# Kernel tuning notes

Hardware: AMD Instinct MI355X
Metric: run time of the kernel (lower is better)

Reference implementation:

```python
import math
import jax, jax.numpy as jnp
from jax import lax
import numpy as np

E = 16        # num experts
K = 2         # top_k
CF = 1.25     # capacity factor


def setup_inputs() -> dict:
    key = jax.random.key(0)
    k0, k1, k2, k3, k4 = jax.random.split(key, 5)
    B, S, D, H = 2, 2048, 1024, 1024
    scale = 0.02
    return {
        "x": jax.random.normal(k0, (B, S, D), dtype=jnp.float32),
        "router_w": jax.random.normal(k1, (D, E), dtype=jnp.float32) * scale,
        "gate_w": jax.random.normal(k2, (E, D, H), dtype=jnp.float32) * scale,
        "up_w": jax.random.normal(k3, (E, D, H), dtype=jnp.float32) * scale,
        "down_w": jax.random.normal(k4, (E, H, D), dtype=jnp.float32) * scale,
    }


def reference(x, router_w, gate_w, up_w, down_w):
    B, S, D = x.shape
    xf = x.reshape(-1, D)                     # [T, D]
    T = B * S
    capacity = max(1, math.ceil(T * K / E * CF))   # static python int
    Cbuf = K * capacity                       # per-expert buffer (per-column capacity x K)

    # ---- router: softmax over experts, then top-k (weights = top-k probs) ----
    logits = xf @ router_w                    # [T, E]
    probs = jax.nn.softmax(logits, axis=-1)
    w, idx = lax.top_k(probs, K)              # [T, K] each

    # ---- capacity drop: per k-column, per expert, keep first `capacity` tokens ----
    oh = jax.nn.one_hot(idx, E, dtype=w.dtype)            # [T, K, E]
    rank = jnp.cumsum(oh, axis=0) - oh                     # exclusive rank per (k, e)
    myrank = jnp.sum(rank * oh, axis=-1)                   # [T, K]
    keep = myrank < capacity
    w = jnp.where(keep, w, 0.0)

    # ---- dispatch: scatter kept assignments into [E, Cbuf] slots ----
    flat_e = idx.reshape(-1)                               # [A], A = T*K (row-major: token-major)
    flat_w = w.reshape(-1)
    keep_f = keep.reshape(-1)
    tok = jnp.repeat(jnp.arange(T, dtype=jnp.int32), K)    # [A]
    ohk = jax.nn.one_hot(flat_e, E, dtype=jnp.int32) * keep_f[:, None].astype(jnp.int32)
    pos = jnp.cumsum(ohk, axis=0) - ohk                    # exclusive rank among kept per expert
    slot = jnp.sum(pos * ohk, axis=-1)                     # [A], < Cbuf for kept
    e_idx = jnp.where(keep_f, flat_e, E)                   # dropped -> dummy expert row E

    dispatch = jnp.full((E + 1, Cbuf), T, dtype=jnp.int32).at[e_idx, slot].set(tok)
    wbuf = jnp.zeros((E + 1, Cbuf), dtype=w.dtype).at[e_idx, slot].set(flat_w)
    dispatch = dispatch[:E]
    wbuf = wbuf[:E]

    x_pad = jnp.concatenate([xf, jnp.zeros((1, D), xf.dtype)], axis=0)  # sentinel row
    xe = x_pad[dispatch]                                   # [E, Cbuf, D]

    # ---- grouped SwiGLU expert GEMMs ----
    gate = jnp.einsum('ecd,edh->ech', xe, gate_w)
    up = jnp.einsum('ecd,edh->ech', xe, up_w)
    hidden = jax.nn.silu(gate) * up
    out = jnp.einsum('ech,ehd->ecd', hidden, down_w)       # [E, Cbuf, D]
    out = out * wbuf[:, :, None]

    # ---- combine: scatter-add back to tokens ----
    combined = jnp.zeros((T + 1, D), dtype=xf.dtype).at[dispatch.reshape(-1)].add(out.reshape(-1, D))
    return combined[:T].reshape(B, S, D)
```

## Files before the change

### kernel.cpp

```cpp
#include <hip/hip_runtime.h>
#include <math.h>

#define T_TOK 4096
#define DIM   1024
#define HID   1024
#define NE    16
#define CAP   640
#define CBUF  1280
#define BM 128
#define BN 64
#define BK 32
#define MAXTILE 160

typedef __attribute__((ext_vector_type(8))) short short8;
typedef __attribute__((ext_vector_type(4))) float f32x4;

static __device__ __forceinline__ unsigned short f2bf(float f) {
    unsigned int u = __float_as_uint(f);
    u += 0x7fff + ((u >> 16) & 1);
    return (unsigned short)(u >> 16);
}

#define PICK4(v,i) ((i)==0?(v).x:(i)==1?(v).y:(i)==2?(v).z:(v).w)

static __device__ __forceinline__ void async16(const void* g, void* l) {
    __builtin_amdgcn_global_load_lds((const __attribute__((address_space(1))) void*)g,
                                     (__attribute__((address_space(3))) void*)l, 16, 0, 0);
}

__global__ void convert_x_k(const float* __restrict__ x, unsigned short* __restrict__ xb) {
    int i = blockIdx.x * blockDim.x + threadIdx.x;
    int base = i * 4;
    int row = base >> 10;
    ushort4 o;
    if (row < T_TOK) {
        float4 v = *(const float4*)(x + base);
        o.x = f2bf(v.x); o.y = f2bf(v.y); o.z = f2bf(v.z); o.w = f2bf(v.w);
    } else {
        o.x = 0; o.y = 0; o.z = 0; o.w = 0;
    }
    *(ushort4*)(xb + base) = o;
}

__global__ void router_k(const float* __restrict__ x, const float* __restrict__ rw,
                         int* __restrict__ route_e, float* __restrict__ route_w) {
    int t = blockIdx.x;
    int lane = threadIdx.x;
    const float* xr = x + (size_t)t * DIM + lane * 16;
    float4 xv0 = *(const float4*)(xr + 0);
    float4 xv1 = *(const float4*)(xr + 4);
    float4 xv2 = *(const float4*)(xr + 8);
    float4 xv3 = *(const float4*)(xr + 12);
    float xl[16] = {xv0.x, xv0.y, xv0.z, xv0.w, xv1.x, xv1.y, xv1.z, xv1.w,
                    xv2.x, xv2.y, xv2.z, xv2.w, xv3.x, xv3.y, xv3.z, xv3.w};
    float p[16];
    #pragma unroll
    for (int e = 0; e < 16; ++e) p[e] = 0.f;
    #pragma unroll
    for (int j = 0; j < 16; ++j) {
        const float4* rp = (const float4*)(rw + (size_t)(lane * 16 + j) * 16);
        float4 r0 = rp[0], r1 = rp[1], r2 = rp[2], r3 = rp[3];
        float xv = xl[j];
        p[0]  += xv * r0.x; p[1]  += xv * r0.y; p[2]  += xv * r0.z; p[3]  += xv * r0.w;
        p[4]  += xv * r1.x; p[5]  += xv * r1.y; p[6]  += xv * r1.z; p[7]  += xv * r1.w;
        p[8]  += xv * r2.x; p[9]  += xv * r2.y; p[10] += xv * r2.z; p[11] += xv * r2.w;
        p[12] += xv * r3.x; p[13] += xv * r3.y; p[14] += xv * r3.z; p[15] += xv * r3.w;
    }
    #pragma unroll
    for (int off = 32; off > 0; off >>= 1) {
        #pragma unroll
        for (int e = 0; e < 16; ++e) p[e] += __shfl_xor(p[e], off);
    }
    if (lane == 0) {
        float m = p[0];
        #pragma unroll
        for (int e = 1; e < 16; ++e) m = fmaxf(m, p[e]);
        float s = 0.f;
        #pragma unroll
        for (int e = 0; e < 16; ++e) s = s + __expf(p[e] - m);
        float v0 = -1e30f, v1 = -1e30f; int i0 = 0, i1 = 0;
        #pragma unroll
        for (int e = 0; e < 16; ++e) {
            float v = p[e];
            if (v > v0)      { v1 = v0; i1 = i0; v0 = v; i0 = e; }
            else if (v > v1) { v1 = v;  i1 = e; }
        }
        route_e[t*2+0] = i0;  route_e[t*2+1] = i1;
        route_w[t*2+0] = __expf(v0 - m) / s;
        route_w[t*2+1] = __expf(v1 - m) / s;
    }
}

__global__ __launch_bounds__(1024)
void build_dispatch_k(const int* __restrict__ route_e, const float* __restrict__ route_w,
                      int* __restrict__ disp, int* __restrict__ smap, int* __restrict__ tmeta) {
    __shared__ unsigned char eidx[2 * T_TOK];
    __shared__ unsigned char keepf[2 * T_TOK];
    __shared__ int totals[NE];
    int tid = threadIdx.x;
    int wv = tid >> 6, lane = tid & 63;

    {
        int4 a = ((const int4*)route_e)[tid * 2];
        int4 b = ((const int4*)route_e)[tid * 2 + 1];
        unsigned int lo = (a.x & 0xff) | ((a.y & 0xff) << 8) | ((a.z & 0xff) << 16) | ((a.w & 0xff) << 24);
        unsigned int hi = (b.x & 0xff) | ((b.y & 0xff) << 8) | ((b.z & 0xff) << 16) | ((b.w & 0xff) << 24);
        uint2 pk; pk.x = lo; pk.y = hi;
        *(uint2*)(eidx + tid * 8) = pk;
    }
    for (int i = tid; i < 2 * T_TOK; i += 1024) smap[i] = -1;
    __syncthreads();

    unsigned long long below = (lane == 0) ? 0ull : ((~0ull) >> (64 - lane));
    #pragma unroll
    for (int s = 0; s < 2; ++s) {
        int st = wv + s * 16;
        int e = st >> 1, k = st & 1;
        int run = 0;
        for (int base = 0; base < T_TOK; base += 64) {
            int t = base + lane;
            int hit = (eidx[t * 2 + k] == e);
            unsigned long long m = __ballot(hit);
            int rank = run + __popcll(m & below);
            if (hit) keepf[t * 2 + k] = (rank < CAP) ? 1 : 0;
            run += __popcll(m);
        }
    }
    __syncthreads();

    {
        int e = wv;
        int run = 0;
        for (int base = 0; base < 2 * T_TOK; base += 64) {
            int f = base + lane;
            int hit = (eidx[f] == e) && keepf[f];
            unsigned long long m = __ballot(hit);
            int slot = run + __popcll(m & below);
            if (hit) {
                disp[e * CBUF + slot] = f >> 1;
                smap[f] = e * CBUF + slot;
            }
            run += __popcll(m);
        }
        if (lane == 0) totals[e] = run;
    }
    __syncthreads();

    for (int i = tid; i < NE * CBUF; i += 1024) {
        int e = i / CBUF, s = i - e * CBUF;
        if (s >= totals[e]) disp[i] = T_TOK;
    }

    if (tid == 0) {
        int n = 0;
        for (int e = 0; e < NE; ++e) {
            int ntl = (totals[e] + BM - 1) / BM;
            for (int m = 0; m < ntl; ++m) { tmeta[4 + n] = (e << 8) | m; ++n; }
        }
        tmeta[0] = n;
    }
}

__global__ __launch_bounds__(256, 2)
void gemm1_k(const unsigned short* __restrict__ xb, const float* __restrict__ gw,
             const float* __restrict__ uw, const int* __restrict__ disp,
             const int* __restrict__ tmeta, unsigned short* __restrict__ hidden) {
    int slot = blockIdx.y;
    if (slot >= tmeta[0]) return;
    int pk = tmeta[4 + slot];
    int e = pk >> 8, mt = pk & 255;
    int m0 = mt * BM, n0 = blockIdx.x * BN;

    __shared__ unsigned short As[2 * BM * BK];
    __shared__ unsigned short Bg[2 * BN * BK];
    __shared__ unsigned short Bu[2 * BN * BK];
    __shared__ int tok[BM];
    int tid = threadIdx.x;
    if (tid < BM) tok[tid] = disp[e * CBUF + m0 + tid];
    __syncthreads();

    int lane = tid & 63, w = tid >> 6;
    int cg = (lane & 3) ^ ((lane >> 3) & 3);
    int rl = lane >> 2;
    int rA0 = w * 32 + rl, rA1 = rA0 + 16;
    const unsigned short* srcA0 = xb + (size_t)tok[rA0] * DIM + cg * 8;
    const unsigned short* srcA1 = xb + (size_t)tok[rA1] * DIM + cg * 8;
    unsigned short* dA0 = As + (w * 32) * BK;
    unsigned short* dA1 = As + (w * 32 + 16) * BK;

    int matb = tid >> 7;
    int kidx = (tid >> 4) & 7;
    int k4 = kidx * 4;
    int g = tid & 15;
    const float* Wsrc = (matb ? uw : gw) + (size_t)e * DIM * HID + (size_t)k4 * HID + n0 + g * 4;
    unsigned short* Bmine = matb ? Bu : Bg;
    int bOff = (((k4 >> 3) ^ (g & 3)) << 3) + ((k4 >> 2) & 1) * 4;

    int wm = w >> 1, wn = w & 1;
    int quad = lane >> 4, ln = lane & 15;
    int swqA = quad ^ ((ln >> 1) & 3);
    int swqB = quad ^ ((ln >> 2) & 3);

    f32x4 zero4 = {0.f, 0.f, 0.f, 0.f};
    f32x4 accg[4][2], accu[4][2];
    #pragma unroll
    for (int i = 0; i < 4; ++i)
        #pragma unroll
        for (int j = 0; j < 2; ++j) { accg[i][j] = zero4; accu[i][j] = zero4; }

    {
        float4 r0 = *(const float4*)(Wsrc);
        float4 r1 = *(const float4*)(Wsrc + 1024);
        float4 r2 = *(const float4*)(Wsrc + 2048);
        float4 r3 = *(const float4*)(Wsrc + 3072);
        async16(srcA0, dA0); async16(srcA1, dA1);
        #pragma unroll
        for (int i = 0; i < 4; ++i) {
            uint2 pkv;
            pkv.x = (unsigned int)f2bf(PICK4(r0, i)) | ((unsigned int)f2bf(PICK4(r1, i)) << 16);
            pkv.y = (unsigned int)f2bf(PICK4(r2, i)) | ((unsigned int)f2bf(PICK4(r3, i)) << 16);
            *(uint2*)(Bmine + (g * 4 + i) * BK + bOff) = pkv;
        }
        asm volatile("s_waitcnt vmcnt(0) lgkmcnt(0)\n\ts_barrier" ::: "memory");
    }

    for (int k0 = 0; k0 < DIM; k0 += BK) {
        int cur = (k0 >> 5) & 1, nx = cur ^ 1;
        float4 r0, r1, r2, r3;
        if (k0 + BK < DIM) {
            const float* Ws = Wsrc + (size_t)(k0 + BK) * 1024;
            r0 = *(const float4*)(Ws);
            r1 = *(const float4*)(Ws + 1024);
            r2 = *(const float4*)(Ws + 2048);
            r3 = *(const float4*)(Ws + 3072);
            async16(srcA0 + k0 + BK, dA0 + nx * (BM * BK));
            async16(srcA1 + k0 + BK, dA1 + nx * (BM * BK));
        }
        const unsigned short* Ab = As + cur * (BM * BK);
        const unsigned short* Gb = Bg + cur * (BN * BK);
        const unsigned short* Ub = Bu + cur * (BN * BK);
        short8 af[4], bgf[2], buf2[2];
        #pragma unroll
        for (int i = 0; i < 4; ++i)
            af[i] = *(const short8*)(Ab + (wm * 64 + i * 16 + ln) * BK + swqA * 8);
        #pragma unroll
        for (int j = 0; j < 2; ++j) {
            bgf[j]  = *(const short8*)(Gb + (wn * 32 + j * 16 + ln) * BK + swqB * 8);
            buf2[j] = *(const short8*)(Ub + (wn * 32 + j * 16 + ln) * BK + swqB * 8);
        }
        #pragma unroll
        for (int i = 0; i < 4; ++i)
            #pragma unroll
            for (int j = 0; j < 2; ++j) {
                accg[i][j] = __builtin_amdgcn_mfma_f32_16x16x32_bf16(af[i], bgf[j],  accg[i][j], 0, 0, 0);
                accu[i][j] = __builtin_amdgcn_mfma_f32_16x16x32_bf16(af[i], buf2[j], accu[i][j], 0, 0, 0);
            }
        if (k0 + BK < DIM) {
            #pragma unroll
            for (int i = 0; i < 4; ++i) {
                uint2 pkv;
                pkv.x = (unsigned int)f2bf(PICK4(r0, i)) | ((unsigned int)f2bf(PICK4(r1, i)) << 16);
                pkv.y = (unsigned int)f2bf(PICK4(r2, i)) | ((unsigned int)f2bf(PICK4(r3, i)) << 16);
                *(uint2*)(Bmine + nx * (BN * BK) + (g * 4 + i) * BK + bOff) = pkv;
            }
        }
        asm volatile("s_waitcnt vmcnt(0) lgkmcnt(0)\n\ts_barrier" ::: "memory");
    }
    #pragma unroll
    for (int i = 0; i < 4; ++i) {
        #pragma unroll
        for (int r = 0; r < 4; ++r) {
            int row = m0 + wm * 64 + i * 16 + quad * 4 + r;
            unsigned short* hrow = hidden + ((size_t)e * CBUF + row) * HID + n0 + wn * 32 + ln;
            #pragma unroll
            for (int j = 0; j < 2; ++j) {
                float gv = accg[i][j][r];
                float uv = accu[i][j][r];
                float sg = gv / (1.f + __expf(-gv));
                hrow[j * 16] = f2bf(sg * uv);
            }
        }
    }
}

__global__ __launch_bounds__(256, 2)
void gemm2_k(const unsigned short* __restrict__ hidden, const float* __restrict__ dw,
             const int* __restrict__ tmeta, unsigned short* __restrict__ ebuf) {
    int slot = blockIdx.y;
    if (slot >= tmeta[0]) return;
    int pk = tmeta[4 + slot];
    int e = pk >> 8, mt = pk & 255;
    int m0 = mt * BM, n0 = blockIdx.x * BN;

    __shared__ unsigned short As[2 * BM * BK];
    __shared__ unsigned short Bs[2 * BN * BK];
    int tid = threadIdx.x;

    int lane = tid & 63, w = tid >> 6;
    int cg = (lane & 3) ^ ((lane >> 3) & 3);
    int rl = lane >> 2;
    int rA0 = w * 32 + rl, rA1 = rA0 + 16;
    const unsigned short* srcA0 = hidden + ((size_t)e * CBUF + m0 + rA0) * HID + cg * 8;
    const unsigned short* srcA1 = hidden + ((size_t)e * CBUF + m0 + rA1) * HID + cg * 8;
    unsigned short* dA0 = As + (w * 32) * BK;
    unsigned short* dA1 = As + (w * 32 + 16) * BK;

    int g2 = tid & 31;
    int kidx2 = ((tid >> 5) & 3) | ((tid >> 7) << 2);
    int k4 = kidx2 * 4;
    const float* Wsrc = dw + (size_t)e * HID * DIM + (size_t)k4 * DIM + n0 + g2 * 2;
    int bOff = (((k4 >> 3) ^ ((g2 >> 1) & 3)) << 3) + ((k4 >> 2) & 1) * 4;

    int wm = w >> 1, wn = w & 1;
    int quad = lane >> 4, ln = lane & 15;
    int swqA = quad ^ ((ln >> 1) & 3);
    int swqB = quad ^ ((ln >> 2) & 3);

    f32x4 zero4 = {0.f, 0.f, 0.f, 0.f};
    f32x4 acc[4][2];
    #pragma unroll
    for (int i = 0; i < 4; ++i)
        #pragma unroll
        for (int j = 0; j < 2; ++j) acc[i][j] = zero4;

    {
        float2 r0 = *(const float2*)(Wsrc);
        float2 r1 = *(const float2*)(Wsrc + 1024);
        float2 r2 = *(const float2*)(Wsrc + 2048);
        float2 r3 = *(const float2*)(Wsrc + 3072);
        async16(srcA0, dA0); async16(srcA1, dA1);
        #pragma unroll
        for (int i = 0; i < 2; ++i) {
            uint2 pkv;
            pkv.x = (unsigned int)f2bf(i ? r0.y : r0.x) | ((unsigned int)f2bf(i ? r1.y : r1.x) << 16);
            pkv.y = (unsigned int)f2bf(i ? r2.y : r2.x) | ((unsigned int)f2bf(i ? r3.y : r3.x) << 16);
            *(uint2*)(Bs + (g2 * 2 + i) * BK + bOff) = pkv;
        }
        asm volatile("s_waitcnt vmcnt(0) lgkmcnt(0)\n\ts_barrier" ::: "memory");
    }

    for (int k0 = 0; k0 < HID; k0 += BK) {
        int cur = (k0 >> 5) & 1, nx = cur ^ 1;
        float2 r0, r1, r2, r3;
        if (k0 + BK < HID) {
            const float* Ws = Wsrc + (size_t)(k0 + BK) * 1024;
            r0 = *(const float2*)(Ws);
            r1 = *(const float2*)(Ws + 1024);
            r2 = *(const float2*)(Ws + 2048);
            r3 = *(const float2*)(Ws + 3072);
            async16(srcA0 + k0 + BK, dA0 + nx * (BM * BK));
            async16(srcA1 + k0 + BK, dA1 + nx * (BM * BK));
        }
        const unsigned short* Ab = As + cur * (BM * BK);
        const unsigned short* Bb = Bs + cur * (BN * BK);
        short8 af[4], bf[2];
        #pragma unroll
        for (int i = 0; i < 4; ++i)
            af[i] = *(const short8*)(Ab + (wm * 64 + i * 16 + ln) * BK + swqA * 8);
        #pragma unroll
        for (int j = 0; j < 2; ++j)
            bf[j] = *(const short8*)(Bb + (wn * 32 + j * 16 + ln) * BK + swqB * 8);
        #pragma unroll
        for (int i = 0; i < 4; ++i)
            #pragma unroll
            for (int j = 0; j < 2; ++j)
                acc[i][j] = __builtin_amdgcn_mfma_f32_16x16x32_bf16(af[i], bf[j], acc[i][j], 0, 0, 0);
        if (k0 + BK < HID) {
            #pragma unroll
            for (int i = 0; i < 2; ++i) {
                uint2 pkv;
                pkv.x = (unsigned int)f2bf(i ? r0.y : r0.x) | ((unsigned int)f2bf(i ? r1.y : r1.x) << 16);
                pkv.y = (unsigned int)f2bf(i ? r2.y : r2.x) | ((unsigned int)f2bf(i ? r3.y : r3.x) << 16);
                *(uint2*)(Bs + nx * (BN * BK) + (g2 * 2 + i) * BK + bOff) = pkv;
            }
        }
        asm volatile("s_waitcnt vmcnt(0) lgkmcnt(0)\n\ts_barrier" ::: "memory");
    }
    #pragma unroll
    for (int i = 0; i < 4; ++i) {
        #pragma unroll
        for (int r = 0; r < 4; ++r) {
            int row = m0 + wm * 64 + i * 16 + quad * 4 + r;
            unsigned short* erow = ebuf + ((size_t)e * CBUF + row) * DIM + n0 + wn * 32 + ln;
            #pragma unroll
            for (int j = 0; j < 2; ++j)
                erow[j * 16] = f2bf(acc[i][j][r]);
        }
    }
}

__global__ __launch_bounds__(256)
void combine_k(const unsigned short* __restrict__ ebuf, const int* __restrict__ smap,
               const float* __restrict__ rwt, float* __restrict__ out) {
    int t = blockIdx.x * 2 + (threadIdx.x >> 7);
    int c = (threadIdx.x & 127) * 8;
    float acc[8];
    #pragma unroll
    for (int j = 0; j < 8; ++j) acc[j] = 0.f;
    #pragma unroll
    for (int k = 0; k < 2; ++k) {
        int sm = smap[t * 2 + k];
        if (sm >= 0) {
            float wgt = rwt[t * 2 + k];
            uint4 rv = *(const uint4*)(ebuf + (size_t)sm * DIM + c);
            unsigned int d[4] = {rv.x, rv.y, rv.z, rv.w};
            #pragma unroll
            for (int q = 0; q < 4; ++q) {
                acc[q * 2 + 0] += wgt * __uint_as_float(d[q] << 16);
                acc[q * 2 + 1] += wgt * __uint_as_float(d[q] & 0xffff0000u);
            }
        }
    }
    float4 o0 = {acc[0], acc[1], acc[2], acc[3]};
    float4 o1 = {acc[4], acc[5], acc[6], acc[7]};
    float* orow = out + (size_t)t * DIM + c;
    *(float4*)(orow + 0) = o0;
    *(float4*)(orow + 4) = o1;
}

extern "C" void kernel_launch(void* const* d_in, const int* in_sizes, int n_in,
                              void* d_out, int out_size, void* d_ws, size_t ws_size,
                              hipStream_t stream) {
    const float* x  = (const float*)d_in[0];
    const float* rw = (const float*)d_in[1];
    const float* gw = (const float*)d_in[2];
    const float* uw = (const float*)d_in[3];
    const float* dw = (const float*)d_in[4];
    float* out = (float*)d_out;

    char* ws = (char*)d_ws;
    size_t off = 0;
    auto alloc = [&](size_t bytes) { void* p = ws + off; off += (bytes + 255) & ~(size_t)255; return p; };
    unsigned short* xb   = (unsigned short*)alloc((size_t)(T_TOK + 1) * DIM * 2);
    unsigned short* hid  = (unsigned short*)alloc((size_t)NE * CBUF * HID * 2);
    unsigned short* ebuf = (unsigned short*)alloc((size_t)NE * CBUF * DIM * 2);
    int*   disp   = (int*)alloc((size_t)NE * CBUF * 4);
    int*   smap   = (int*)alloc((size_t)T_TOK * 2 * 4);
    int*   tmeta  = (int*)alloc((4 + MAXTILE) * 4);
    int*   re     = (int*)alloc((size_t)T_TOK * 2 * 4);
    float* rwt    = (float*)alloc((size_t)T_TOK * 2 * 4);
    (void)ws_size; (void)in_sizes; (void)n_in;

    convert_x_k<<<T_TOK + 1, 256, 0, stream>>>(x, xb);
    router_k<<<T_TOK, 64, 0, stream>>>(x, rw, re, rwt);
    build_dispatch_k<<<1, 1024, 0, stream>>>(re, rwt, disp, smap, tmeta);
    gemm1_k<<<dim3(HID / BN, MAXTILE), 256, 0, stream>>>(xb, gw, uw, disp, tmeta, hid);
    gemm2_k<<<dim3(DIM / BN, MAXTILE), 256, 0, stream>>>(hid, dw, tmeta, ebuf);
    combine_k<<<T_TOK / 2, 256, 0, stream>>>(ebuf, smap, rwt, out);
}
```

Measured before the change: 419.8 us.

## Prefetch fp32 weights two stages ahead with partial vmcnt waits in expert GEMMs

Both expert GEMM kernels now load the fp32 weight tile for step k+2 into registers while step k computes. The previous tile is converted to bf16 and written into LDS before the MFMAs rather than after them. Barriers wait with vmcnt(4) so the in-flight weight prefetch is not drained each iteration, and sched_barrier pins the instruction order. Conversion also switches to the packed hardware bf16x2 intrinsic. This hides global-load latency at the cost of more live registers and a fragile dependence on the vmcnt accounting order.

New measurement: 400.2 us. 4.7% less time.

```diff
diff --git a/kernel.cpp b/kernel.cpp
--- a/kernel.cpp
+++ b/kernel.cpp
@@ -1,4 +1,5 @@
 #include <hip/hip_runtime.h>
+#include <hip/hip_bf16.h>
 #include <math.h>
 
 #define T_TOK 4096
@@ -19,6 +20,12 @@
     unsigned int u = __float_as_uint(f);
     u += 0x7fff + ((u >> 16) & 1);
     return (unsigned short)(u >> 16);
+}
+
+static __device__ __forceinline__ unsigned int pack2bf(float lo, float hi) {
+    union { __hip_bfloat162 h; unsigned int u; } cv;
+    cv.h = __float22bfloat162_rn(make_float2(lo, hi));
+    return cv.u;
 }
 
 #define PICK4(v,i) ((i)==0?(v).x:(i)==1?(v).y:(i)==2?(v).z:(v).w)
@@ -208,37 +215,57 @@
         #pragma unroll
         for (int j = 0; j < 2; ++j) { accg[i][j] = zero4; accu[i][j] = zero4; }
 
+    float4 p0, p1, p2, p3;
+
+    p0 = *(const float4*)(Wsrc);
+    p1 = *(const float4*)(Wsrc + 1024);
+    p2 = *(const float4*)(Wsrc + 2048);
+    p3 = *(const float4*)(Wsrc + 3072);
+    async16(srcA0, dA0); async16(srcA1, dA1);
+    __builtin_amdgcn_sched_barrier(0);
+    #pragma unroll
+    for (int i = 0; i < 4; ++i) {
+        uint2 pkv;
+        pkv.x = pack2bf(PICK4(p0, i), PICK4(p1, i));
+        pkv.y = pack2bf(PICK4(p2, i), PICK4(p3, i));
+        *(uint2*)(Bmine + (g * 4 + i) * BK + bOff) = pkv;
+    }
     {
-        float4 r0 = *(const float4*)(Wsrc);
-        float4 r1 = *(const float4*)(Wsrc + 1024);
-        float4 r2 = *(const float4*)(Wsrc + 2048);
-        float4 r3 = *(const float4*)(Wsrc + 3072);
-        async16(srcA0, dA0); async16(srcA1, dA1);
-        #pragma unroll
-        for (int i = 0; i < 4; ++i) {
-            uint2 pkv;
-            pkv.x = (unsigned int)f2bf(PICK4(r0, i)) | ((unsigned int)f2bf(PICK4(r1, i)) << 16);
-            pkv.y = (unsigned int)f2bf(PICK4(r2, i)) | ((unsigned int)f2bf(PICK4(r3, i)) << 16);
-            *(uint2*)(Bmine + (g * 4 + i) * BK + bOff) = pkv;
-        }
-        asm volatile("s_waitcnt vmcnt(0) lgkmcnt(0)\n\ts_barrier" ::: "memory");
-    }
+        const float* Ws = Wsrc + (size_t)BK * 1024;
+        p0 = *(const float4*)(Ws);
+        p1 = *(const float4*)(Ws + 1024);
+        p2 = *(const float4*)(Ws + 2048);
+        p3 = *(const float4*)(Ws + 3072);
+    }
+    asm volatile("s_waitcnt vmcnt(4) lgkmcnt(0)\n\ts_barrier" ::: "memory");
 
     for (int k0 = 0; k0 < DIM; k0 += BK) {
         int cur = (k0 >> 5) & 1, nx = cur ^ 1;
-        float4 r0, r1, r2, r3;
-        if (k0 + BK < DIM) {
-            const float* Ws = Wsrc + (size_t)(k0 + BK) * 1024;
-            r0 = *(const float4*)(Ws);
-            r1 = *(const float4*)(Ws + 1024);
-            r2 = *(const float4*)(Ws + 2048);
-            r3 = *(const float4*)(Ws + 3072);
-            async16(srcA0 + k0 + BK, dA0 + nx * (BM * BK));
-            async16(srcA1 + k0 + BK, dA1 + nx * (BM * BK));
-        }
         const unsigned short* Ab = As + cur * (BM * BK);
         const unsigned short* Gb = Bg + cur * (BN * BK);
         const unsigned short* Ub = Bu + cur * (BN * BK);
+
+        if (k0 + BK < DIM) {
+            #pragma unroll
+            for (int i = 0; i < 4; ++i) {
+                uint2 pkv;
+                pkv.x = pack2bf(PICK4(p0, i), PICK4(p1, i));
+                pkv.y = pack2bf(PICK4(p2, i), PICK4(p3, i));
+                *(uint2*)(Bmine + nx * (BN * BK) + (g * 4 + i) * BK + bOff) = pkv;
+            }
+            async16(srcA0 + k0 + BK, dA0 + nx * (BM * BK));
+            async16(srcA1 + k0 + BK, dA1 + nx * (BM * BK));
+            __builtin_amdgcn_sched_barrier(0);
+            if (k0 + 2 * BK < DIM) {
+                const float* Ws = Wsrc + (size_t)(k0 + 2 * BK) * 1024;
+                p0 = *(const float4*)(Ws);
+                p1 = *(const float4*)(Ws + 1024);
+                p2 = *(const float4*)(Ws + 2048);
+                p3 = *(const float4*)(Ws + 3072);
+                __builtin_amdgcn_sched_barrier(0);
+            }
+        }
+
         short8 af[4], bgf[2], buf2[2];
         #pragma unroll
         for (int i = 0; i < 4; ++i)
@@ -255,16 +282,13 @@
                 accg[i][j] = __builtin_amdgcn_mfma_f32_16x16x32_bf16(af[i], bgf[j],  accg[i][j], 0, 0, 0);
                 accu[i][j] = __builtin_amdgcn_mfma_f32_16x16x32_bf16(af[i], buf2[j], accu[i][j], 0, 0, 0);
             }
+
         if (k0 + BK < DIM) {
-            #pragma unroll
-            for (int i = 0; i < 4; ++i) {
-                uint2 pkv;
-                pkv.x = (unsigned int)f2bf(PICK4(r0, i)) | ((unsigned int)f2bf(PICK4(r1, i)) << 16);
-                pkv.y = (unsigned int)f2bf(PICK4(r2, i)) | ((unsigned int)f2bf(PICK4(r3, i)) << 16);
-                *(uint2*)(Bmine + nx * (BN * BK) + (g * 4 + i) * BK + bOff) = pkv;
-            }
-        }
-        asm volatile("s_waitcnt vmcnt(0) lgkmcnt(0)\n\ts_barrier" ::: "memory");
+            if (k0 + 2 * BK < DIM)
+                asm volatile("s_waitcnt vmcnt(4) lgkmcnt(0)\n\ts_barrier" ::: "memory");
+            else
+                asm volatile("s_waitcnt vmcnt(0) lgkmcnt(0)\n\ts_barrier" ::: "memory");
+        }
     }
     #pragma unroll
     for (int i = 0; i < 4; ++i) {
@@ -323,36 +347,56 @@
         #pragma unroll
         for (int j = 0; j < 2; ++j) acc[i][j] = zero4;
 
+    float2 p0, p1, p2, p3;
+
+    p0 = *(const float2*)(Wsrc);
+    p1 = *(const float2*)(Wsrc + 1024);
+    p2 = *(const float2*)(Wsrc + 2048);
+    p3 = *(const float2*)(Wsrc + 3072);
+    async16(srcA0, dA0); async16(srcA1, dA1);
+    __builtin_amdgcn_sched_barrier(0);
+    #pragma unroll
+    for (int i = 0; i < 2; ++i) {
+        uint2 pkv;
+        pkv.x = pack2bf(i ? p0.y : p0.x, i ? p1.y : p1.x);
+        pkv.y = pack2bf(i ? p2.y : p2.x, i ? p3.y : p3.x);
+        *(uint2*)(Bs + (g2 * 2 + i) * BK + bOff) = pkv;
+    }
     {
-        float2 r0 = *(const float2*)(Wsrc);
-        float2 r1 = *(const float2*)(Wsrc + 1024);
-        float2 r2 = *(const float2*)(Wsrc + 2048);
-        float2 r3 = *(const float2*)(Wsrc + 3072);
-        async16(srcA0, dA0); async16(srcA1, dA1);
-        #pragma unroll
-        for (int i = 0; i < 2; ++i) {
-            uint2 pkv;
-            pkv.x = (unsigned int)f2bf(i ? r0.y : r0.x) | ((unsigned int)f2bf(i ? r1.y : r1.x) << 16);
-            pkv.y = (unsigned int)f2bf(i ? r2.y : r2.x) | ((unsigned int)f2bf(i ? r3.y : r3.x) << 16);
-            *(uint2*)(Bs + (g2 * 2 + i) * BK + bOff) = pkv;
-        }
-        asm volatile("s_waitcnt vmcnt(0) lgkmcnt(0)\n\ts_barrier" ::: "memory");
-    }
+        const float* Ws = Wsrc + (size_t)BK * 1024;
+        p0 = *(const float2*)(Ws);
+        p1 = *(const float2*)(Ws + 1024);
+        p2 = *(const float2*)(Ws + 2048);
+        p3 = *(const float2*)(Ws + 3072);
+    }
+    asm volatile("s_waitcnt vmcnt(4) lgkmcnt(0)\n\ts_barrier" ::: "memory");
 
     for (int k0 = 0; k0 < HID; k0 += BK) {
         int cur = (k0 >> 5) & 1, nx = cur ^ 1;
-        float2 r0, r1, r2, r3;
+        const unsigned short* Ab = As + cur * (BM * BK);
+        const unsigned short* Bb = Bs + cur * (BN * BK);
+
         if (k0 + BK < HID) {
-            const float* Ws = Wsrc + (size_t)(k0 + BK) * 1024;
-            r0 = *(const float2*)(Ws);
-            r1 = *(const float2*)(Ws + 1024);
-            r2 = *(const float2*)(Ws + 2048);
-            r3 = *(const float2*)(Ws + 3072);
+            #pragma unroll
+            for (int i = 0; i < 2; ++i) {
+                uint2 pkv;
+                pkv.x = pack2bf(i ? p0.y : p0.x, i ? p1.y : p1.x);
+                pkv.y = pack2bf(i ? p2.y : p2.x, i ? p3.y : p3.x);
+                *(uint2*)(Bs + nx * (BN * BK) + (g2 * 2 + i) * BK + bOff) = pkv;
+            }
             async16(srcA0 + k0 + BK, dA0 + nx * (BM * BK));
             async16(srcA1 + k0 + BK, dA1 + nx * (BM * BK));
-        }
-        const unsigned short* Ab = As + cur * (BM * BK);
-        const unsigned short* Bb = Bs + cur * (BN * BK);
+            __builtin_amdgcn_sched_barrier(0);
+            if (k0 + 2 * BK < HID) {
+                const float* Ws = Wsrc + (size_t)(k0 + 2 * BK) * 1024;
+                p0 = *(const float2*)(Ws);
+                p1 = *(const float2*)(Ws + 1024);
+                p2 = *(const float2*)(Ws + 2048);
+                p3 = *(const float2*)(Ws + 3072);
+                __builtin_amdgcn_sched_barrier(0);
+            }
+        }
+
         short8 af[4], bf[2];
         #pragma unroll
         for (int i = 0; i < 4; ++i)
@@ -365,16 +409,13 @@
             #pragma unroll
             for (int j = 0; j < 2; ++j)
                 acc[i][j] = __builtin_amdgcn_mfma_f32_16x16x32_bf16(af[i], bf[j], acc[i][j], 0, 0, 0);
+
         if (k0 + BK < HID) {
-            #pragma unroll
-            for (int i = 0; i < 2; ++i) {
-                uint2 pkv;
-                pkv.x = (unsigned int)f2bf(i ? r0.y : r0.x) | ((unsigned int)f2bf(i ? r1.y : r1.x) << 16);
-                pkv.y = (unsigned int)f2bf(i ? r2.y : r2.x) | ((unsigned int)f2bf(i ? r3.y : r3.x) << 16);
-                *(uint2*)(Bs + nx * (BN * BK) + (g2 * 2 + i) * BK + bOff) = pkv;
-            }
-        }
-        asm volatile("s_waitcnt vmcnt(0) lgkmcnt(0)\n\ts_barrier" ::: "memory");
+            if (k0 + 2 * BK < HID)
+                asm volatile("s_waitcnt vmcnt(4) lgkmcnt(0)\n\ts_barrier" ::: "memory");
+            else
+                asm volatile("s_waitcnt vmcnt(0) lgkmcnt(0)\n\ts_barrier" ::: "memory");
+        }
     }
     #pragma unroll
     for (int i = 0; i < 4; ++i) {
```

## Deepen GEMM pipelines with triple-buffered A tiles and two-stage weight prefetch

Applied to the files above, without the earlier changes.

Both expert GEMM kernels now triple-buffer the async A-tile loads to LDS and keep fp32 weight prefetches two K-steps ahead in registers. Partial vmcnt waits replace the full drains at each barrier, so global loads stay in flight across iterations. Weight conversion uses the packed bf16x2 intrinsic, and the token index staging through shared memory with its extra sync is dropped. The cost is more LDS and more registers, which could reduce occupancy, and the hand-counted vmcnt values must match the actual outstanding loads for correctness.

After: 402.4 us. 4.1% less time.

```diff
diff --git a/kernel.cpp b/kernel.cpp
--- a/kernel.cpp
+++ b/kernel.cpp
@@ -1,4 +1,5 @@
 #include <hip/hip_runtime.h>
+#include <hip/hip_bf16.h>
 #include <math.h>
 
 #define T_TOK 4096
@@ -19,6 +20,12 @@
     unsigned int u = __float_as_uint(f);
     u += 0x7fff + ((u >> 16) & 1);
     return (unsigned short)(u >> 16);
+}
+
+static __device__ __forceinline__ unsigned int pack2bf(float lo, float hi) {
+    union { __hip_bfloat162 h; unsigned int u; } cv;
+    cv.h = __float22bfloat162_rn(make_float2(lo, hi));
+    return cv.u;
 }
 
 #define PICK4(v,i) ((i)==0?(v).x:(i)==1?(v).y:(i)==2?(v).z:(v).w)
@@ -171,22 +178,21 @@
     int e = pk >> 8, mt = pk & 255;
     int m0 = mt * BM, n0 = blockIdx.x * BN;
 
-    __shared__ unsigned short As[2 * BM * BK];
+    __shared__ unsigned short As[3 * BM * BK];
     __shared__ unsigned short Bg[2 * BN * BK];
     __shared__ unsigned short Bu[2 * BN * BK];
-    __shared__ int tok[BM];
     int tid = threadIdx.x;
-    if (tid < BM) tok[tid] = disp[e * CBUF + m0 + tid];
-    __syncthreads();
-
     int lane = tid & 63, w = tid >> 6;
+
     int cg = (lane & 3) ^ ((lane >> 3) & 3);
     int rl = lane >> 2;
     int rA0 = w * 32 + rl, rA1 = rA0 + 16;
-    const unsigned short* srcA0 = xb + (size_t)tok[rA0] * DIM + cg * 8;
-    const unsigned short* srcA1 = xb + (size_t)tok[rA1] * DIM + cg * 8;
-    unsigned short* dA0 = As + (w * 32) * BK;
-    unsigned short* dA1 = As + (w * 32 + 16) * BK;
+    int t0 = disp[e * CBUF + m0 + rA0];
+    int t1 = disp[e * CBUF + m0 + rA1];
+    const unsigned short* srcA0 = xb + (size_t)t0 * DIM + cg * 8;
+    const unsigned short* srcA1 = xb + (size_t)t1 * DIM + cg * 8;
+    int dAoff0 = (w * 32) * BK;
+    int dAoff1 = (w * 32 + 16) * BK;
 
     int matb = tid >> 7;
     int kidx = (tid >> 4) & 7;
@@ -208,64 +214,108 @@
         #pragma unroll
         for (int j = 0; j < 2; ++j) { accg[i][j] = zero4; accu[i][j] = zero4; }
 
+    float4 s0_0, s0_1, s0_2, s0_3;
+    float4 s1_0, s1_1, s1_2, s1_3;
+
+    async16(srcA0, As + dAoff0);
+    async16(srcA1, As + dAoff1);
+    async16(srcA0 + BK, As + BM * BK + dAoff0);
+    async16(srcA1 + BK, As + BM * BK + dAoff1);
+    __builtin_amdgcn_sched_barrier(0);
     {
-        float4 r0 = *(const float4*)(Wsrc);
-        float4 r1 = *(const float4*)(Wsrc + 1024);
-        float4 r2 = *(const float4*)(Wsrc + 2048);
-        float4 r3 = *(const float4*)(Wsrc + 3072);
-        async16(srcA0, dA0); async16(srcA1, dA1);
+        float4 a0 = *(const float4*)(Wsrc);
+        float4 a1 = *(const float4*)(Wsrc + 1024);
+        float4 a2 = *(const float4*)(Wsrc + 2048);
+        float4 a3 = *(const float4*)(Wsrc + 3072);
         #pragma unroll
         for (int i = 0; i < 4; ++i) {
             uint2 pkv;
-            pkv.x = (unsigned int)f2bf(PICK4(r0, i)) | ((unsigned int)f2bf(PICK4(r1, i)) << 16);
-            pkv.y = (unsigned int)f2bf(PICK4(r2, i)) | ((unsigned int)f2bf(PICK4(r3, i)) << 16);
+            pkv.x = pack2bf(PICK4(a0, i), PICK4(a1, i));
+            pkv.y = pack2bf(PICK4(a2, i), PICK4(a3, i));
             *(uint2*)(Bmine + (g * 4 + i) * BK + bOff) = pkv;
         }
-        asm volatile("s_waitcnt vmcnt(0) lgkmcnt(0)\n\ts_barrier" ::: "memory");
-    }
-
-    for (int k0 = 0; k0 < DIM; k0 += BK) {
-        int cur = (k0 >> 5) & 1, nx = cur ^ 1;
-        float4 r0, r1, r2, r3;
-        if (k0 + BK < DIM) {
-            const float* Ws = Wsrc + (size_t)(k0 + BK) * 1024;
-            r0 = *(const float4*)(Ws);
-            r1 = *(const float4*)(Ws + 1024);
-            r2 = *(const float4*)(Ws + 2048);
-            r3 = *(const float4*)(Ws + 3072);
-            async16(srcA0 + k0 + BK, dA0 + nx * (BM * BK));
-            async16(srcA1 + k0 + BK, dA1 + nx * (BM * BK));
-        }
-        const unsigned short* Ab = As + cur * (BM * BK);
-        const unsigned short* Gb = Bg + cur * (BN * BK);
-        const unsigned short* Ub = Bu + cur * (BN * BK);
-        short8 af[4], bgf[2], buf2[2];
-        #pragma unroll
-        for (int i = 0; i < 4; ++i)
-            af[i] = *(const short8*)(Ab + (wm * 64 + i * 16 + ln) * BK + swqA * 8);
-        #pragma unroll
-        for (int j = 0; j < 2; ++j) {
-            bgf[j]  = *(const short8*)(Gb + (wn * 32 + j * 16 + ln) * BK + swqB * 8);
-            buf2[j] = *(const short8*)(Ub + (wn * 32 + j * 16 + ln) * BK + swqB * 8);
-        }
-        #pragma unroll
-        for (int i = 0; i < 4; ++i)
-            #pragma unroll
-            for (int j = 0; j < 2; ++j) {
-                accg[i][j] = __builtin_amdgcn_mfma_f32_16x16x32_bf16(af[i], bgf[j],  accg[i][j], 0, 0, 0);
-                accu[i][j] = __builtin_amdgcn_mfma_f32_16x16x32_bf16(af[i], buf2[j], accu[i][j], 0, 0, 0);
-            }
-        if (k0 + BK < DIM) {
-            #pragma unroll
-            for (int i = 0; i < 4; ++i) {
-                uint2 pkv;
-                pkv.x = (unsigned int)f2bf(PICK4(r0, i)) | ((unsigned int)f2bf(PICK4(r1, i)) << 16);
-                pkv.y = (unsigned int)f2bf(PICK4(r2, i)) | ((unsigned int)f2bf(PICK4(r3, i)) << 16);
-                *(uint2*)(Bmine + nx * (BN * BK) + (g * 4 + i) * BK + bOff) = pkv;
-            }
-        }
-        asm volatile("s_waitcnt vmcnt(0) lgkmcnt(0)\n\ts_barrier" ::: "memory");
-    }
+    }
+    __builtin_amdgcn_sched_barrier(0);
+    {
+        const float* W1 = Wsrc + (size_t)BK * 1024;
+        s0_0 = *(const float4*)(W1);
+        s0_1 = *(const float4*)(W1 + 1024);
+        s0_2 = *(const float4*)(W1 + 2048);
+        s0_3 = *(const float4*)(W1 + 3072);
+        const float* W2 = Wsrc + (size_t)(2 * BK) * 1024;
+        s1_0 = *(const float4*)(W2);
+        s1_1 = *(const float4*)(W2 + 1024);
+        s1_2 = *(const float4*)(W2 + 2048);
+        s1_3 = *(const float4*)(W2 + 3072);
+    }
+    __builtin_amdgcn_sched_barrier(0);
+    asm volatile("s_waitcnt lgkmcnt(0)\n\ts_barrier" ::: "memory");
+
+    int aR = 0, aN = BM * BK, aW = 2 * BM * BK;
+
+#define G1_ITER(kk, P0, P1, P2, P3)                                                  \
+    {                                                                                \
+        int curb = (((kk) >> 5) & 1) * (BN * BK);                                    \
+        int nxb  = ((((kk) >> 5) + 1) & 1) * (BN * BK);                              \
+        if ((kk) < DIM - BK) {       \
+            _Pragma("unroll")                                                        \
+            for (int i = 0; i < 4; ++i) {                                            \
+                uint2 pkv;                                                           \
+                pkv.x = pack2bf(PICK4(P0, i), PICK4(P1, i));                         \
+                pkv.y = pack2bf(PICK4(P2, i), PICK4(P3, i));                         \
+                *(uint2*)(Bmine + nxb + (g * 4 + i) * BK + bOff) = pkv;              \
+            }                                                                        \
+        }                                                                            \
+        __builtin_amdgcn_sched_barrier(0);                                           \
+        if ((kk) + 2 * BK < DIM) {            \
+            async16(srcA0 + (kk) + 2 * BK, As + aW + dAoff0);                        \
+            async16(srcA1 + (kk) + 2 * BK, As + aW + dAoff1);                        \
+        }                                                                            \
+        __builtin_amdgcn_sched_barrier(0);                                           \
+        if ((kk) + 3 * BK < DIM) {       \
+            const float* Ws = Wsrc + (size_t)((kk) + 3 * BK) * 1024;                 \
+            P0 = *(const float4*)(Ws);                                               \
+            P1 = *(const float4*)(Ws + 1024);                                        \
+            P2 = *(const float4*)(Ws + 2048);                                        \
+            P3 = *(const float4*)(Ws + 3072);                                        \
+        }                                                                            \
+        __builtin_amdgcn_sched_barrier(0);                                           \
+        {                                                                            \
+            const unsigned short* Ab = As + aR;                                      \
+            const unsigned short* Gb = Bg + curb;                                    \
+            const unsigned short* Ub = Bu + curb;                                    \
+            short8 af[4], bgf[2], buf2[2];                                           \
+            _Pragma("unroll")                                                        \
+            for (int i = 0; i < 4; ++i)                                              \
+                af[i] = *(const short8*)(Ab + (wm * 64 + i * 16 + ln) * BK + swqA * 8); \
+            _Pragma("unroll")                                                        \
+            for (int j = 0; j < 2; ++j) {                                            \
+                bgf[j]  = *(const short8*)(Gb + (wn * 32 + j * 16 + ln) * BK + swqB * 8); \
+                buf2[j] = *(const short8*)(Ub + (wn * 32 + j * 16 + ln) * BK + swqB * 8); \
+            }                                                                        \
+            _Pragma("unroll")                                                        \
+            for (int i = 0; i < 4; ++i)                                              \
+                _Pragma("unroll")                                                    \
+                for (int j = 0; j < 2; ++j) {                                        \
+                    accg[i][j] = __builtin_amdgcn_mfma_f32_16x16x32_bf16(af[i], bgf[j],  accg[i][j], 0, 0, 0); \
+                    accu[i][j] = __builtin_amdgcn_mfma_f32_16x16x32_bf16(af[i], buf2[j], accu[i][j], 0, 0, 0); \
+                }                                                                    \
+        }                                                                            \
+        if ((kk) + 3 * BK < DIM)                                                     \
+            asm volatile("s_waitcnt vmcnt(10) lgkmcnt(0)\n\ts_barrier" ::: "memory"); \
+        else if ((kk) + 2 * BK < DIM)                                                \
+            asm volatile("s_waitcnt vmcnt(6) lgkmcnt(0)\n\ts_barrier" ::: "memory");  \
+        else                                                                         \
+            asm volatile("s_waitcnt vmcnt(0) lgkmcnt(0)\n\ts_barrier" ::: "memory");  \
+        { int _t = aR; aR = aN; aN = aW; aW = _t; }                                  \
+    }
+
+    for (int k0 = 0; k0 < DIM; k0 += 2 * BK) {
+        G1_ITER(k0,      s0_0, s0_1, s0_2, s0_3);
+        G1_ITER(k0 + BK, s1_0, s1_1, s1_2, s1_3);
+    }
+#undef G1_ITER
+
     #pragma unroll
     for (int i = 0; i < 4; ++i) {
         #pragma unroll
@@ -292,18 +342,18 @@
     int e = pk >> 8, mt = pk & 255;
     int m0 = mt * BM, n0 = blockIdx.x * BN;
 
-    __shared__ unsigned short As[2 * BM * BK];
+    __shared__ unsigned short As[3 * BM * BK];
     __shared__ unsigned short Bs[2 * BN * BK];
     int tid = threadIdx.x;
-
     int lane = tid & 63, w = tid >> 6;
+
     int cg = (lane & 3) ^ ((lane >> 3) & 3);
     int rl = lane >> 2;
     int rA0 = w * 32 + rl, rA1 = rA0 + 16;
     const unsigned short* srcA0 = hidden + ((size_t)e * CBUF + m0 + rA0) * HID + cg * 8;
     const unsigned short* srcA1 = hidden + ((size_t)e * CBUF + m0 + rA1) * HID + cg * 8;
-    unsigned short* dA0 = As + (w * 32) * BK;
-    unsigned short* dA1 = As + (w * 32 + 16) * BK;
+    int dAoff0 = (w * 32) * BK;
+    int dAoff1 = (w * 32 + 16) * BK;
 
     int g2 = tid & 31;
     int kidx2 = ((tid >> 5) & 3) | ((tid >> 7) << 2);
@@ -323,59 +373,103 @@
         #pragma unroll
         for (int j = 0; j < 2; ++j) acc[i][j] = zero4;
 
+    float2 s0_0, s0_1, s0_2, s0_3;
+    float2 s1_0, s1_1, s1_2, s1_3;
+
+    async16(srcA0, As + dAoff0);
+    async16(srcA1, As + dAoff1);
+    async16(srcA0 + BK, As + BM * BK + dAoff0);
+    async16(srcA1 + BK, As + BM * BK + dAoff1);
+    __builtin_amdgcn_sched_barrier(0);
     {
-        float2 r0 = *(const float2*)(Wsrc);
-        float2 r1 = *(const float2*)(Wsrc + 1024);
-        float2 r2 = *(const float2*)(Wsrc + 2048);
-        float2 r3 = *(const float2*)(Wsrc + 3072);
-        async16(srcA0, dA0); async16(srcA1, dA1);
+        float2 a0 = *(const float2*)(Wsrc);
+        float2 a1 = *(const float2*)(Wsrc + 1024);
+        float2 a2 = *(const float2*)(Wsrc + 2048);
+        float2 a3 = *(const float2*)(Wsrc + 3072);
         #pragma unroll
         for (int i = 0; i < 2; ++i) {
             uint2 pkv;
-            pkv.x = (unsigned int)f2bf(i ? r0.y : r0.x) | ((unsigned int)f2bf(i ? r1.y : r1.x) << 16);
-            pkv.y = (unsigned int)f2bf(i ? r2.y : r2.x) | ((unsigned int)f2bf(i ? r3.y : r3.x) << 16);
+            pkv.x = pack2bf(i ? a0.y : a0.x, i ? a1.y : a1.x);
+            pkv.y = pack2bf(i ? a2.y : a2.x, i ? a3.y : a3.x);
             *(uint2*)(Bs + (g2 * 2 + i) * BK + bOff) = pkv;
         }
-        asm volatile("s_waitcnt vmcnt(0) lgkmcnt(0)\n\ts_barrier" ::: "memory");
-    }
-
-    for (int k0 = 0; k0 < HID; k0 += BK) {
-        int cur = (k0 >> 5) & 1, nx = cur ^ 1;
-        float2 r0, r1, r2, r3;
-        if (k0 + BK < HID) {
-            const float* Ws = Wsrc + (size_t)(k0 + BK) * 1024;
-            r0 = *(const float2*)(Ws);
-            r1 = *(const float2*)(Ws + 1024);
-            r2 = *(const float2*)(Ws + 2048);
-            r3 = *(const float2*)(Ws + 3072);
-            async16(srcA0 + k0 + BK, dA0 + nx * (BM * BK));
-            async16(srcA1 + k0 + BK, dA1 + nx * (BM * BK));
-        }
-        const unsigned short* Ab = As + cur * (BM * BK);
-        const unsigned short* Bb = Bs + cur * (BN * BK);
-        short8 af[4], bf[2];
-        #pragma unroll
-        for (int i = 0; i < 4; ++i)
-            af[i] = *(const short8*)(Ab + (wm * 64 + i * 16 + ln) * BK + swqA * 8);
-        #pragma unroll
-        for (int j = 0; j < 2; ++j)
-            bf[j] = *(const short8*)(Bb + (wn * 32 + j * 16 + ln) * BK + swqB * 8);
-        #pragma unroll
-        for (int i = 0; i < 4; ++i)
-            #pragma unroll
-            for (int j = 0; j < 2; ++j)
-                acc[i][j] = __builtin_amdgcn_mfma_f32_16x16x32_bf16(af[i], bf[j], acc[i][j], 0, 0, 0);
-        if (k0 + BK < HID) {
-            #pragma unroll
-            for (int i = 0; i < 2; ++i) {
-                uint2 pkv;
-                pkv.x = (unsigned int)f2bf(i ? r0.y : r0.x) | ((unsigned int)f2bf(i ? r1.y : r1.x) << 16);
-                pkv.y = (unsigned int)f2bf(i ? r2.y : r2.x) | ((unsigned int)f2bf(i ? r3.y : r3.x) << 16);
-                *(uint2*)(Bs + nx * (BN * BK) + (g2 * 2 + i) * BK + bOff) = pkv;
-            }
-        }
-        asm volatile("s_waitcnt vmcnt(0) lgkmcnt(0)\n\ts_barrier" ::: "memory");
-    }
+    }
+    __builtin_amdgcn_sched_barrier(0);
+    {
+        const float* W1 = Wsrc + (size_t)BK * 1024;
+        s0_0 = *(const float2*)(W1);
+        s0_1 = *(const float2*)(W1 + 1024);
+        s0_2 = *(const float2*)(W1 + 2048);
+        s0_3 = *(const float2*)(W1 + 3072);
+        const float* W2 = Wsrc + (size_t)(2 * BK) * 1024;
+        s1_0 = *(const float2*)(W2);
+        s1_1 = *(const float2*)(W2 + 1024);
+        s1_2 = *(const float2*)(W2 + 2048);
+        s1_3 = *(const float2*)(W2 + 3072);
+    }
+    __builtin_amdgcn_sched_barrier(0);
+    asm volatile("s_waitcnt lgkmcnt(0)\n\ts_barrier" ::: "memory");
+
+    int aR = 0, aN = BM * BK, aW = 2 * BM * BK;
+
+#define G2_ITER(kk, P0, P1, P2, P3)                                                  \
+    {                                                                                \
+        int curb = (((kk) >> 5) & 1) * (BN * BK);                                    \
+        int nxb  = ((((kk) >> 5) + 1) & 1) * (BN * BK);                              \
+        if ((kk) < HID - BK) {                                                       \
+            _Pragma("unroll")                                                        \
+            for (int i = 0; i < 2; ++i) {                                            \
+                uint2 pkv;                                                           \
+                pkv.x = pack2bf(i ? P0.y : P0.x, i ? P1.y : P1.x);                   \
+                pkv.y = pack2bf(i ? P2.y : P2.x, i ? P3.y : P3.x);                   \
+                *(uint2*)(Bs + nxb + (g2 * 2 + i) * BK + bOff) = pkv;                \
+            }                                                                        \
+        }                                                                            \
+        __builtin_amdgcn_sched_barrier(0);                                           \
+        if ((kk) + 2 * BK < HID) {                                                   \
+            async16(srcA0 + (kk) + 2 * BK, As + aW + dAoff0);                        \
+            async16(srcA1 + (kk) + 2 * BK, As + aW + dAoff1);                        \
+        }                                                                            \
+        __builtin_amdgcn_sched_barrier(0);                                           \
+        if ((kk) + 3 * BK < HID) {                                                   \
+            const float* Ws = Wsrc + (size_t)((kk) + 3 * BK) * 1024;                 \
+            P0 = *(const float2*)(Ws);                                               \
+            P1 = *(const float2*)(Ws + 1024);                                        \
+            P2 = *(const float2*)(Ws + 2048);                                        \
+            P3 = *(const float2*)(Ws + 3072);                                        \
+        }                                                                            \
+        __builtin_amdgcn_sched_barrier(0);                                           \
+        {                                                                            \
+            const unsigned short* Ab = As + aR;                                      \
+            const unsigned short* Bb = Bs + curb;                                    \
+            short8 af[4], bf[2];                                                     \
+            _Pragma("unroll")                                                        \
+            for (int i = 0; i < 4; ++i)                                              \
+                af[i] = *(const short8*)(Ab + (wm * 64 + i * 16 + ln) * BK + swqA * 8); \
+            _Pragma("unroll")                                                        \
+            for (int j = 0; j < 2; ++j)                                              \
+                bf[j] = *(const short8*)(Bb + (wn * 32 + j * 16 + ln) * BK + swqB * 8); \
+            _Pragma("unroll")                                                        \
+            for (int i = 0; i < 4; ++i)                                              \
+                _Pragma("unroll")                                                    \
+                for (int j = 0; j < 2; ++j)                                          \
+                    acc[i][j] = __builtin_amdgcn_mfma_f32_16x16x32_bf16(af[i], bf[j], acc[i][j], 0, 0, 0); \
+        }                                                                            \
+        if ((kk) + 3 * BK < HID)                                                     \
+            asm volatile("s_waitcnt vmcnt(10) lgkmcnt(0)\n\ts_barrier" ::: "memory"); \
+        else if ((kk) + 2 * BK < HID)                                                \
+            asm volatile("s_waitcnt vmcnt(6) lgkmcnt(0)\n\ts_barrier" ::: "memory");  \
+        else                                                                         \
+            asm volatile("s_waitcnt vmcnt(0) lgkmcnt(0)\n\ts_barrier" ::: "memory");  \
+        { int _t = aR; aR = aN; aN = aW; aW = _t; }                                  \
+    }
+
+    for (int k0 = 0; k0 < HID; k0 += 2 * BK) {
+        G2_ITER(k0,      s0_0, s0_1, s0_2, s0_3);
+        G2_ITER(k0 + BK, s1_0, s1_1, s1_2, s1_3);
+    }
+#undef G2_ITER
+
     #pragma unroll
     for (int i = 0; i < 4; ++i) {
         #pragma unroll
```
